# Kernel tuning notes

Measured on AMD Instinct MI355X. Metric: run time of the kernel, lower is better.

Reference implementation:

```python
import jax, jax.numpy as jnp
import numpy as np

N = 100000   # nodes
E = 1600000  # edges
D = 128      # input feature dim
H = 64       # hidden dim
G = 64       # graphs in batch


def setup_inputs() -> dict:
    key = jax.random.key(0)
    ks = jax.random.split(key, 12)
    x = jax.random.normal(ks[0], (N, D), dtype=jnp.float32)
    ei = jax.random.randint(ks[1], (2, E), 0, N, dtype=jnp.int32)
    ew = jax.random.uniform(ks[2], (E,), dtype=jnp.float32)
    b = jnp.sort(jax.random.randint(ks[3], (N,), 0, G, dtype=jnp.int32))
    s = 0.05
    W1 = jax.random.normal(ks[4], (D, H), jnp.float32) * s
    b1 = jnp.zeros((H,), jnp.float32)
    W2 = jax.random.normal(ks[5], (H, H), jnp.float32) * s
    b2 = jnp.zeros((H,), jnp.float32)
    Wm1 = jax.random.normal(ks[6], (H, 32), jnp.float32) * s
    bm1 = jnp.zeros((32,), jnp.float32)
    Wm2 = jax.random.normal(ks[7], (32, 1), jnp.float32) * s
    bm2 = jnp.zeros((1,), jnp.float32)
    return {"x": x, "ei": ei, "ew": ew, "b": b,
            "W1": W1, "b1": b1, "W2": W2, "b2": b2,
            "Wm1": Wm1, "bm1": bm1, "Wm2": Wm2, "bm2": bm2}


def _gcn_norm(ei, ew, n):
    # PyG gcn_norm with add_self_loops=True (self-loop weight 1)
    loops = jnp.arange(n, dtype=ei.dtype)
    row = jnp.concatenate([ei[0], loops])
    col = jnp.concatenate([ei[1], loops])
    w = jnp.concatenate([ew, jnp.ones((n,), ew.dtype)])
    deg = jax.ops.segment_sum(w, col, num_segments=n)
    dinv = jnp.where(deg > 0, jax.lax.rsqrt(deg), 0.0)
    norm = dinv[row] * w * dinv[col]  # [E+N]
    return row, col, norm


def _gcn_conv(x, W, bias, row, col, norm, n):
    h = x @ W                                   # [N,H] small GEMM
    msg = h[row] * norm[:, None]                # gather over edges
    return jax.ops.segment_sum(msg, col, num_segments=n) + bias


def reference(x, ei, ew, b, W1, b1, W2, b2, Wm1, bm1, Wm2, bm2):
    n = x.shape[0]
    row, col, norm = _gcn_norm(ei, ew, n)
    h = jax.nn.relu(_gcn_conv(x, W1, b1, row, col, norm, n))
    h = jax.nn.relu(_gcn_conv(h, W2, b2, row, col, norm, n))
    # global_mean_pool over batch vector b
    sums = jax.ops.segment_sum(h, b, num_segments=G)
    cnt = jax.ops.segment_sum(jnp.ones((n,), h.dtype), b, num_segments=G)
    pooled = sums / jnp.maximum(cnt, 1.0)[:, None]  # [G,H]
    # MLP head: Linear(H,32) -> ReLU -> Linear(32,1)
    return jax.nn.relu(pooled @ Wm1 + bm1) @ Wm2 + bm2
```

## Files before the change

kernel.cpp:

```cpp
#include <hip/hip_runtime.h>
#include <hip/hip_bf16.h>
#include <hip/hip_fp16.h>


#define DIMH 64
#define BSH 7
#define BSZ 128
#define NBUCK_MAX 1024
#define EPB 4096
#define ESTRIDE 3072
#define CSTRIDE 4096

typedef _Float16 v8h __attribute__((ext_vector_type(8)));
typedef _Float16 v4h __attribute__((ext_vector_type(4)));
typedef _Float16 hv2 __attribute__((ext_vector_type(2)));
typedef float v4f __attribute__((ext_vector_type(4)));

__global__ __launch_bounds__(512) void k_part(const int* __restrict__ row,
                                              const int* __restrict__ col,
                                              const float* __restrict__ ew,
                                              int* __restrict__ cursor,
                                              unsigned long long* __restrict__ part,
                                              int E, int nbuck) {
    __shared__ int h[NBUCK_MAX];
    __shared__ int h2[NBUCK_MAX];
    __shared__ int st[NBUCK_MAX];
    for (int i = threadIdx.x; i < nbuck; i += 512) { h[i] = 0; h2[i] = 0; }
    __syncthreads();
    int ebeg = blockIdx.x * EPB;
    int eend = min(ebeg + EPB, E);
    for (int e = ebeg + threadIdx.x; e < eend; e += 512)
        atomicAdd(&h[col[e] >> BSH], 1);
    __syncthreads();
    for (int i = threadIdx.x; i < nbuck; i += 512) {
        int c = h[i];
        st[i] = c ? i * ESTRIDE + atomicAdd(&cursor[i], c) : 0;
    }
    __syncthreads();
    for (int e = ebeg + threadIdx.x; e < eend; e += 512) {
        int c = col[e];
        int b = c >> BSH;
        int r = atomicAdd(&h2[b], 1);
        int slot = st[b] + r;
        if (slot < (b + 1) * ESTRIDE) {
            unsigned long long rec =
                ((unsigned long long)__float_as_uint(ew[e]) << 32) |
                ((unsigned long long)(unsigned)row[e] << 8) |
                (unsigned)(c & (BSZ - 1));
            part[slot] = rec;
        }
    }
}

__global__ __launch_bounds__(256) void k_sortB(const unsigned long long* __restrict__ part,
                                               const int* __restrict__ cursor,
                                               int2* __restrict__ csr,
                                               unsigned* __restrict__ rp,
                                               float* __restrict__ dinv, int N) {
    __shared__ int cnt[BSZ];
    __shared__ int scn[BSZ];
    __shared__ int cur[BSZ];
    __shared__ float dg[BSZ];
    int b = blockIdx.x;
    int nb0 = b << BSH;
    int nn = min(BSZ, N - nb0);
    int tid = threadIdx.x;
    if (tid < BSZ) { cnt[tid] = 0; dg[tid] = 1.0f; }
    __syncthreads();
    int ebeg = b * ESTRIDE;
    int eend = ebeg + min(cursor[b], ESTRIDE);
    for (int e = ebeg + tid; e < eend; e += 256)
        atomicAdd(&cnt[(int)(part[e] & (BSZ - 1))], 1);
    __syncthreads();
    int pc = 0;
    if (tid < BSZ) pc = min((cnt[tid] + 15) & ~15, 496);
    if (tid < BSZ) scn[tid] = pc;
    __syncthreads();
    for (int o = 1; o < BSZ; o <<= 1) {
        int t = 0;
        if (tid >= o && tid < BSZ) t = scn[tid - o];
        __syncthreads();
        if (tid >= o && tid < BSZ) scn[tid] += t;
        __syncthreads();
    }
    int Pb = b * CSTRIDE;
    int pofs = 0;
    if (tid < BSZ) {
        pofs = scn[tid] - pc;
        cur[tid] = pofs;
        if (tid < nn)
            rp[nb0 + tid] = ((unsigned)(pc >> 4) << 26) | (unsigned)(Pb + pofs);
    }
    __syncthreads();
    for (int e = ebeg + tid; e < eend; e += 256) {
        unsigned long long rec = part[e];
        int cl = (int)(rec & (BSZ - 1));
        float w = __uint_as_float((unsigned)(rec >> 32));
        int slot = atomicAdd(&cur[cl], 1);
        csr[Pb + slot] = make_int2((int)((rec >> 8) & 0xFFFFFF), __float_as_int(w));
        atomicAdd(&dg[cl], w);
    }
    __syncthreads();
    if (tid < nn) {
        int c = min(cnt[tid], pc);
        for (int k = c; k < pc; k++)
            csr[Pb + pofs + k] = make_int2(nb0 + tid, 0);
        dinv[nb0 + tid] = rsqrtf(dg[tid]);
    }
}

__global__ __launch_bounds__(256) void k_gemm_mfma(const float* __restrict__ X,
                                                   const float* __restrict__ W,
                                                   const float* __restrict__ dinv,
                                                   __half* __restrict__ Y, int n) {
    __shared__ _Float16 Wh[128 * 64];
    int tid = threadIdx.x;
    for (int i = tid * 4; i < 128 * 64; i += 256 * 4) {
        float4 w = *(const float4*)&W[i];
        Wh[i]     = (_Float16)w.x;
        Wh[i + 1] = (_Float16)w.y;
        Wh[i + 2] = (_Float16)w.z;
        Wh[i + 3] = (_Float16)w.w;
    }
    __syncthreads();

    int wv = tid >> 6;
    int lane = tid & 63;
    int m = lane & 15;
    int quad = lane >> 4;
    int tile = blockIdx.x * 4 + wv;
    int ntiles = (n + 15) >> 4;
    if (tile >= ntiles) return;

    v8h bf[4][4];
#pragma unroll
    for (int nt = 0; nt < 4; nt++)
#pragma unroll
        for (int s = 0; s < 4; s++)
#pragma unroll
            for (int j = 0; j < 8; j++)
                bf[nt][s][j] = Wh[(s * 32 + quad * 8 + j) * 64 + nt * 16 + m];

    v4f acc[4];
#pragma unroll
    for (int nt = 0; nt < 4; nt++) acc[nt] = (v4f){0.f, 0.f, 0.f, 0.f};

    int row = min(tile * 16 + m, n - 1);
    const float* xr = X + (size_t)row * 128;
#pragma unroll
    for (int s = 0; s < 4; s++) {
        float4 lo = *(const float4*)&xr[s * 32 + quad * 8];
        float4 hi = *(const float4*)&xr[s * 32 + quad * 8 + 4];
        v8h af;
        af[0] = (_Float16)lo.x; af[1] = (_Float16)lo.y;
        af[2] = (_Float16)lo.z; af[3] = (_Float16)lo.w;
        af[4] = (_Float16)hi.x; af[5] = (_Float16)hi.y;
        af[6] = (_Float16)hi.z; af[7] = (_Float16)hi.w;
#pragma unroll
        for (int nt = 0; nt < 4; nt++)
            acc[nt] = __builtin_amdgcn_mfma_f32_16x16x32_f16(af, bf[nt][s], acc[nt], 0, 0, 0);
    }

#pragma unroll
    for (int r = 0; r < 4; r++) {
        int node = tile * 16 + quad * 4 + r;
        if (node < n) {
            float di = dinv[node];
#pragma unroll
            for (int nt = 0; nt < 4; nt++)
                Y[(size_t)node * DIMH + nt * 16 + m] = __float2half(di * acc[nt][r]);
        }
    }
}

__global__ __launch_bounds__(256, 8) void k_agg1f(const __half* __restrict__ Hin,
                                                  const unsigned* __restrict__ rp,
                                                  const int2* __restrict__ csr,
                                                  const float* __restrict__ dinv,
                                                  const float* __restrict__ bias,
                                                  const float* __restrict__ W2,
                                                  __half* __restrict__ T2, int n) {
    __shared__ __align__(16) _Float16 W2T[64 * 68];
    __shared__ __align__(16) _Float16 hbuf[4][DIMH];
    int tid = threadIdx.x;
    for (int idx = tid; idx < 64 * 64; idx += 256) {
        int k = idx >> 6;
        int o = idx & 63;
        W2T[o * 68 + k] = (_Float16)W2[idx];
    }
    __syncthreads();

    int lane = tid & 63;
    int wv = tid >> 6;
    int q = lane >> 4;
    int fp = lane & 15;

    const char* Hb = (const char*)Hin;
    const char* Cb = (const char*)csr;
    int ngroups = (n + 3) >> 2;
    for (int grp = blockIdx.x; grp < ngroups; grp += gridDim.x) {
        int node = grp * 4 + wv;
        if (node >= n) continue;
        unsigned pk = rp[node];
        unsigned pb = ((pk & 0x3FFFFFFu) << 3) + (unsigned)(q << 4);
        int iters = (int)(pk >> 26);
        float a0 = 0.f, a1 = 0.f, a2 = 0.f, a3 = 0.f;
        if (q == 0) {
            uint2 su = *(const uint2*)(Hb + (((unsigned)node << 7) + (unsigned)(fp << 3)));
            float2 f0 = __half22float2(*(__half2*)&su.x);
            float2 f1 = __half22float2(*(__half2*)&su.y);
            a0 = f0.x; a1 = f0.y; a2 = f1.x; a3 = f1.y;
        }
        unsigned fo = (unsigned)(fp << 3);
        int it = 0;
        for (; it + 2 <= iters; it += 2, pb += 256) {
            int4 mA0 = *(const int4*)(Cb + pb);
            int4 mB0 = *(const int4*)(Cb + pb + 64);
            int4 mA1 = *(const int4*)(Cb + pb + 128);
            int4 mB1 = *(const int4*)(Cb + pb + 192);
            uint2 u0 = *(const uint2*)(Hb + (((unsigned)mA0.x << 7) + fo));
            uint2 u1 = *(const uint2*)(Hb + (((unsigned)mA0.z << 7) + fo));
            uint2 u2 = *(const uint2*)(Hb + (((unsigned)mB0.x << 7) + fo));
            uint2 u3 = *(const uint2*)(Hb + (((unsigned)mB0.z << 7) + fo));
            uint2 u4 = *(const uint2*)(Hb + (((unsigned)mA1.x << 7) + fo));
            uint2 u5 = *(const uint2*)(Hb + (((unsigned)mA1.z << 7) + fo));
            uint2 u6 = *(const uint2*)(Hb + (((unsigned)mB1.x << 7) + fo));
            uint2 u7 = *(const uint2*)(Hb + (((unsigned)mB1.z << 7) + fo));
            float w0 = __int_as_float(mA0.y), w1 = __int_as_float(mA0.w);
            float w2 = __int_as_float(mB0.y), w3 = __int_as_float(mB0.w);
            float w4 = __int_as_float(mA1.y), w5 = __int_as_float(mA1.w);
            float w6 = __int_as_float(mB1.y), w7 = __int_as_float(mB1.w);
            float2 f;
            f = __half22float2(*(__half2*)&u0.x); a0 += w0 * f.x; a1 += w0 * f.y;
            f = __half22float2(*(__half2*)&u0.y); a2 += w0 * f.x; a3 += w0 * f.y;
            f = __half22float2(*(__half2*)&u1.x); a0 += w1 * f.x; a1 += w1 * f.y;
            f = __half22float2(*(__half2*)&u1.y); a2 += w1 * f.x; a3 += w1 * f.y;
            f = __half22float2(*(__half2*)&u2.x); a0 += w2 * f.x; a1 += w2 * f.y;
            f = __half22float2(*(__half2*)&u2.y); a2 += w2 * f.x; a3 += w2 * f.y;
            f = __half22float2(*(__half2*)&u3.x); a0 += w3 * f.x; a1 += w3 * f.y;
            f = __half22float2(*(__half2*)&u3.y); a2 += w3 * f.x; a3 += w3 * f.y;
            f = __half22float2(*(__half2*)&u4.x); a0 += w4 * f.x; a1 += w4 * f.y;
            f = __half22float2(*(__half2*)&u4.y); a2 += w4 * f.x; a3 += w4 * f.y;
            f = __half22float2(*(__half2*)&u5.x); a0 += w5 * f.x; a1 += w5 * f.y;
            f = __half22float2(*(__half2*)&u5.y); a2 += w5 * f.x; a3 += w5 * f.y;
            f = __half22float2(*(__half2*)&u6.x); a0 += w6 * f.x; a1 += w6 * f.y;
            f = __half22float2(*(__half2*)&u6.y); a2 += w6 * f.x; a3 += w6 * f.y;
            f = __half22float2(*(__half2*)&u7.x); a0 += w7 * f.x; a1 += w7 * f.y;
            f = __half22float2(*(__half2*)&u7.y); a2 += w7 * f.x; a3 += w7 * f.y;
        }
        if (it < iters) {
            int4 mA = *(const int4*)(Cb + pb);
            int4 mB = *(const int4*)(Cb + pb + 64);
            uint2 u0 = *(const uint2*)(Hb + (((unsigned)mA.x << 7) + fo));
            uint2 u1 = *(const uint2*)(Hb + (((unsigned)mA.z << 7) + fo));
            uint2 u2 = *(const uint2*)(Hb + (((unsigned)mB.x << 7) + fo));
            uint2 u3 = *(const uint2*)(Hb + (((unsigned)mB.z << 7) + fo));
            float w0 = __int_as_float(mA.y), w1 = __int_as_float(mA.w);
            float w2 = __int_as_float(mB.y), w3 = __int_as_float(mB.w);
            float2 f;
            f = __half22float2(*(__half2*)&u0.x); a0 += w0 * f.x; a1 += w0 * f.y;
            f = __half22float2(*(__half2*)&u0.y); a2 += w0 * f.x; a3 += w0 * f.y;
            f = __half22float2(*(__half2*)&u1.x); a0 += w1 * f.x; a1 += w1 * f.y;
            f = __half22float2(*(__half2*)&u1.y); a2 += w1 * f.x; a3 += w1 * f.y;
            f = __half22float2(*(__half2*)&u2.x); a0 += w2 * f.x; a1 += w2 * f.y;
            f = __half22float2(*(__half2*)&u2.y); a2 += w2 * f.x; a3 += w2 * f.y;
            f = __half22float2(*(__half2*)&u3.x); a0 += w3 * f.x; a1 += w3 * f.y;
            f = __half22float2(*(__half2*)&u3.y); a2 += w3 * f.x; a3 += w3 * f.y;
        }
        a0 += __shfl_xor(a0, 16, 64); a0 += __shfl_xor(a0, 32, 64);
        a1 += __shfl_xor(a1, 16, 64); a1 += __shfl_xor(a1, 32, 64);
        a2 += __shfl_xor(a2, 16, 64); a2 += __shfl_xor(a2, 32, 64);
        a3 += __shfl_xor(a3, 16, 64); a3 += __shfl_xor(a3, 32, 64);
        float di = dinv[node];
        if (q == 0) {
            float4 bs = *(const float4*)&bias[fp * 4];
            float v0 = fmaxf(di * a0 + bs.x, 0.f);
            float v1 = fmaxf(di * a1 + bs.y, 0.f);
            float v2 = fmaxf(di * a2 + bs.z, 0.f);
            float v3 = fmaxf(di * a3 + bs.w, 0.f);
            __half2 h0 = __floats2half2_rn(v0, v1);
            __half2 h1 = __floats2half2_rn(v2, v3);
            uint2 o;
            o.x = *(unsigned*)&h0;
            o.y = *(unsigned*)&h1;
            *(uint2*)&hbuf[wv][fp * 4] = o;
        }
        float accA = 0.f, accB = 0.f;
#pragma unroll
        for (int k8 = 0; k8 < 8; k8++) {
            v8h hv = *(const v8h*)&hbuf[wv][k8 * 8];
            v4h wa = *(const v4h*)&W2T[lane * 68 + k8 * 8];
            v4h wb = *(const v4h*)&W2T[lane * 68 + k8 * 8 + 4];
            hv2 h0 = {hv[0], hv[1]}, h1 = {hv[2], hv[3]};
            hv2 h2_ = {hv[4], hv[5]}, h3 = {hv[6], hv[7]};
            hv2 w0 = {wa[0], wa[1]}, w1 = {wa[2], wa[3]};
            hv2 w2_ = {wb[0], wb[1]}, w3 = {wb[2], wb[3]};
            accA = __builtin_amdgcn_fdot2(h0, w0, accA, false);
            accB = __builtin_amdgcn_fdot2(h1, w1, accB, false);
            accA = __builtin_amdgcn_fdot2(h2_, w2_, accA, false);
            accB = __builtin_amdgcn_fdot2(h3, w3, accB, false);
        }
        T2[(size_t)node * DIMH + lane] = __float2half(di * (accA + accB));
    }
}

__global__ __launch_bounds__(256, 8) void k_aggN(const __half* __restrict__ Hin,
                                                 const unsigned* __restrict__ rp,
                                                 const int2* __restrict__ csr,
                                                 const float* __restrict__ dinv,
                                                 const float* __restrict__ bias,
                                                 __half* __restrict__ Hout, int n) {
    int lane = threadIdx.x & 63;
    int wv = threadIdx.x >> 6;
    int node = blockIdx.x * 4 + wv;
    if (node >= n) return;
    unsigned pk = rp[node];
    int iters = (int)(pk >> 26);
    int q = lane >> 4;
    int fp = lane & 15;
    unsigned pb = ((pk & 0x3FFFFFFu) << 3) + (unsigned)(q << 4);
    unsigned fo = (unsigned)(fp << 3);
    const char* Hb = (const char*)Hin;
    const char* Cb = (const char*)csr;
    float a0 = 0.f, a1 = 0.f, a2 = 0.f, a3 = 0.f;
    if (q == 0) {
        uint2 su = *(const uint2*)(Hb + (((unsigned)node << 7) + fo));
        float2 f0 = __half22float2(*(__half2*)&su.x);
        float2 f1 = __half22float2(*(__half2*)&su.y);
        a0 = f0.x; a1 = f0.y; a2 = f1.x; a3 = f1.y;
    }
    int it = 0;
    for (; it + 2 <= iters; it += 2, pb += 256) {
        int4 mA0 = *(const int4*)(Cb + pb);
        int4 mB0 = *(const int4*)(Cb + pb + 64);
        int4 mA1 = *(const int4*)(Cb + pb + 128);
        int4 mB1 = *(const int4*)(Cb + pb + 192);
        uint2 u0 = *(const uint2*)(Hb + (((unsigned)mA0.x << 7) + fo));
        uint2 u1 = *(const uint2*)(Hb + (((unsigned)mA0.z << 7) + fo));
        uint2 u2 = *(const uint2*)(Hb + (((unsigned)mB0.x << 7) + fo));
        uint2 u3 = *(const uint2*)(Hb + (((unsigned)mB0.z << 7) + fo));
        uint2 u4 = *(const uint2*)(Hb + (((unsigned)mA1.x << 7) + fo));
        uint2 u5 = *(const uint2*)(Hb + (((unsigned)mA1.z << 7) + fo));
        uint2 u6 = *(const uint2*)(Hb + (((unsigned)mB1.x << 7) + fo));
        uint2 u7 = *(const uint2*)(Hb + (((unsigned)mB1.z << 7) + fo));
        float w0 = __int_as_float(mA0.y), w1 = __int_as_float(mA0.w);
        float w2 = __int_as_float(mB0.y), w3 = __int_as_float(mB0.w);
        float w4 = __int_as_float(mA1.y), w5 = __int_as_float(mA1.w);
        float w6 = __int_as_float(mB1.y), w7 = __int_as_float(mB1.w);
        float2 f;
        f = __half22float2(*(__half2*)&u0.x); a0 += w0 * f.x; a1 += w0 * f.y;
        f = __half22float2(*(__half2*)&u0.y); a2 += w0 * f.x; a3 += w0 * f.y;
        f = __half22float2(*(__half2*)&u1.x); a0 += w1 * f.x; a1 += w1 * f.y;
        f = __half22float2(*(__half2*)&u1.y); a2 += w1 * f.x; a3 += w1 * f.y;
        f = __half22float2(*(__half2*)&u2.x); a0 += w2 * f.x; a1 += w2 * f.y;
        f = __half22float2(*(__half2*)&u2.y); a2 += w2 * f.x; a3 += w2 * f.y;
        f = __half22float2(*(__half2*)&u3.x); a0 += w3 * f.x; a1 += w3 * f.y;
        f = __half22float2(*(__half2*)&u3.y); a2 += w3 * f.x; a3 += w3 * f.y;
        f = __half22float2(*(__half2*)&u4.x); a0 += w4 * f.x; a1 += w4 * f.y;
        f = __half22float2(*(__half2*)&u4.y); a2 += w4 * f.x; a3 += w4 * f.y;
        f = __half22float2(*(__half2*)&u5.x); a0 += w5 * f.x; a1 += w5 * f.y;
        f = __half22float2(*(__half2*)&u5.y); a2 += w5 * f.x; a3 += w5 * f.y;
        f = __half22float2(*(__half2*)&u6.x); a0 += w6 * f.x; a1 += w6 * f.y;
        f = __half22float2(*(__half2*)&u6.y); a2 += w6 * f.x; a3 += w6 * f.y;
        f = __half22float2(*(__half2*)&u7.x); a0 += w7 * f.x; a1 += w7 * f.y;
        f = __half22float2(*(__half2*)&u7.y); a2 += w7 * f.x; a3 += w7 * f.y;
    }
    if (it < iters) {
        int4 mA = *(const int4*)(Cb + pb);
        int4 mB = *(const int4*)(Cb + pb + 64);
        uint2 u0 = *(const uint2*)(Hb + (((unsigned)mA.x << 7) + fo));
        uint2 u1 = *(const uint2*)(Hb + (((unsigned)mA.z << 7) + fo));
        uint2 u2 = *(const uint2*)(Hb + (((unsigned)mB.x << 7) + fo));
        uint2 u3 = *(const uint2*)(Hb + (((unsigned)mB.z << 7) + fo));
        float w0 = __int_as_float(mA.y), w1 = __int_as_float(mA.w);
        float w2 = __int_as_float(mB.y), w3 = __int_as_float(mB.w);
        float2 f;
        f = __half22float2(*(__half2*)&u0.x); a0 += w0 * f.x; a1 += w0 * f.y;
        f = __half22float2(*(__half2*)&u0.y); a2 += w0 * f.x; a3 += w0 * f.y;
        f = __half22float2(*(__half2*)&u1.x); a0 += w1 * f.x; a1 += w1 * f.y;
        f = __half22float2(*(__half2*)&u1.y); a2 += w1 * f.x; a3 += w1 * f.y;
        f = __half22float2(*(__half2*)&u2.x); a0 += w2 * f.x; a1 += w2 * f.y;
        f = __half22float2(*(__half2*)&u2.y); a2 += w2 * f.x; a3 += w2 * f.y;
        f = __half22float2(*(__half2*)&u3.x); a0 += w3 * f.x; a1 += w3 * f.y;
        f = __half22float2(*(__half2*)&u3.y); a2 += w3 * f.x; a3 += w3 * f.y;
    }
    a0 += __shfl_xor(a0, 16, 64); a0 += __shfl_xor(a0, 32, 64);
    a1 += __shfl_xor(a1, 16, 64); a1 += __shfl_xor(a1, 32, 64);
    a2 += __shfl_xor(a2, 16, 64); a2 += __shfl_xor(a2, 32, 64);
    a3 += __shfl_xor(a3, 16, 64); a3 += __shfl_xor(a3, 32, 64);
    if (q == 0) {
        float di = dinv[node];
        float4 bs = *(const float4*)&bias[fp * 4];
        float v0 = fmaxf(di * a0 + bs.x, 0.f);
        float v1 = fmaxf(di * a1 + bs.y, 0.f);
        float v2 = fmaxf(di * a2 + bs.z, 0.f);
        float v3 = fmaxf(di * a3 + bs.w, 0.f);
        __half2 h0 = __floats2half2_rn(v0, v1);
        __half2 h1 = __floats2half2_rn(v2, v3);
        uint2 o;
        o.x = *(unsigned*)&h0;
        o.y = *(unsigned*)&h1;
        *(uint2*)&Hout[(size_t)node * DIMH + fp * 4] = o;
    }
}

__global__ __launch_bounds__(256) void k_pool(const __half* __restrict__ Hin,
                                              const int* __restrict__ b,
                                              float* __restrict__ sums,
                                              float* __restrict__ cntG, int n) {
    const int CHUNK = 64;
    int lane = threadIdx.x & 63;
    int wave = threadIdx.x >> 6;
    int start = (blockIdx.x * 4 + wave) * CHUNK;
    if (start >= n) return;
    int end = min(start + CHUNK, n);
    float acc = 0.f;
    int g_cur = b[start];
    int cnt_local = 0;
    for (int i = start; i < end; i++) {
        int g = b[i];
        if (g != g_cur) {
            atomicAdd(&sums[g_cur * DIMH + lane], acc);
            if (lane == 0) atomicAdd(&cntG[g_cur], (float)cnt_local);
            acc = 0.f;
            cnt_local = 0;
            g_cur = g;
        }
        acc += __half2float(Hin[(size_t)i * DIMH + lane]);
        cnt_local++;
    }
    atomicAdd(&sums[g_cur * DIMH + lane], acc);
    if (lane == 0) atomicAdd(&cntG[g_cur], (float)cnt_local);
}

__global__ __launch_bounds__(64) void k_mlp(const float* __restrict__ sums,
                                            const float* __restrict__ cntG,
                                            const float* __restrict__ Wm1,
                                            const float* __restrict__ bm1,
                                            const float* __restrict__ Wm2,
                                            const float* __restrict__ bm2,
                                            float* __restrict__ out, int G) {
    int g = threadIdx.x;
    if (g >= G) return;
    float c = cntG[g];
    float inv = 1.f / (c > 1.f ? c : 1.f);
    float pooled[DIMH];
#pragma unroll
    for (int k = 0; k < DIMH; k++) pooled[k] = sums[g * DIMH + k] * inv;
    float o = 0.f;
    for (int j = 0; j < 32; j++) {
        float t = bm1[j];
#pragma unroll
        for (int k = 0; k < DIMH; k++) t += pooled[k] * Wm1[k * 32 + j];
        t = t > 0.f ? t : 0.f;
        o += t * Wm2[j];
    }
    out[g] = o + bm2[0];
}


extern "C" void kernel_launch(void* const* d_in, const int* in_sizes, int n_in,
                              void* d_out, int out_size, void* d_ws, size_t ws_size,
                              hipStream_t stream) {
    const float* x   = (const float*)d_in[0];
    const int*   ei  = (const int*)d_in[1];
    const float* ew  = (const float*)d_in[2];
    const int*   bvec= (const int*)d_in[3];
    const float* W1  = (const float*)d_in[4];
    const float* b1  = (const float*)d_in[5];
    const float* W2  = (const float*)d_in[6];
    const float* b2  = (const float*)d_in[7];
    const float* Wm1 = (const float*)d_in[8];
    const float* bm1 = (const float*)d_in[9];
    const float* Wm2 = (const float*)d_in[10];
    const float* bm2 = (const float*)d_in[11];
    float* out = (float*)d_out;

    const int E = in_sizes[2];
    const int N = in_sizes[3];
    const int G = out_size;
    const int* row = ei;
    const int* col = ei + E;
    const int nbuck = (N + BSZ - 1) >> BSH;

    char* p = (char*)d_ws;
    auto alloc = [&](size_t bytes) {
        void* r = (void*)p;
        p += (bytes + 255) & ~(size_t)255;
        return r;
    };

    unsigned long long* part = (unsigned long long*)alloc((size_t)nbuck * ESTRIDE * 8);
    int2*  csr    = (int2*)alloc((size_t)nbuck * CSTRIDE * 8);
    unsigned* rp  = (unsigned*)alloc((size_t)N * 4);
    float* dinv   = (float*)alloc((size_t)N * 4);
    __half* hA    = (__half*)alloc((size_t)N * DIMH * 2);
    __half* hB    = (__half*)alloc((size_t)N * DIMH * 2);
    int zeroInts  = nbuck + G * DIMH + G;
    int* cursor   = (int*)alloc((size_t)zeroInts * 4);
    float* sums   = (float*)(cursor + nbuck);
    float* cntG   = sums + G * DIMH;

    hipMemsetAsync(cursor, 0, (size_t)zeroInts * 4, stream);

    const int PB = (E + EPB - 1) / EPB;
    const int NT = (N + 15) / 16;

    k_part<<<PB, 512, 0, stream>>>(row, col, ew, cursor, part, E, nbuck);
    k_sortB<<<nbuck, 256, 0, stream>>>(part, cursor, csr, rp, dinv, N);

    k_gemm_mfma<<<(NT + 3) / 4, 256, 0, stream>>>(x, W1, dinv, hA, N);

    k_agg1f<<<4096, 256, 0, stream>>>(hA, rp, csr, dinv, b1, W2, hB, N);

    k_aggN<<<(N + 3) / 4, 256, 0, stream>>>(hB, rp, csr, dinv, b2, hA, N);

    k_pool<<<(N + 255) / 256, 256, 0, stream>>>(hA, bvec, sums, cntG, N);
    k_mlp<<<1, 64, 0, stream>>>(sums, cntG, Wm1, bm1, Wm2, bm2, out, G);
}
```

Before: 312.6 us.

## Split layer-2 features into four column planes and aggregate each plane separately

k_agg1f now writes the transformed layer-2 features in a planar layout: four 16-feature planes of 32-byte rows instead of 128-byte rows. The second aggregation kernel launches a 4-wide grid in y, one plane per y index, and each wave gathers 32-byte chunks with 16 edge groups of 4 lanes. The aim is for each plane (3.2 MB) to fit in cache so the random gathers hit better. In exchange the CSR edge list is read four times, and there are two more shuffle-reduction stages and smaller per-lane gathers.

```diff
diff --git a/kernel.cpp b/kernel.cpp
--- a/kernel.cpp
+++ b/kernel.cpp
@@ -300,97 +300,71 @@
             accA = __builtin_amdgcn_fdot2(h2_, w2_, accA, false);
             accB = __builtin_amdgcn_fdot2(h3, w3, accB, false);
         }
-        T2[(size_t)node * DIMH + lane] = __float2half(di * (accA + accB));
-    }
-}
-
-__global__ __launch_bounds__(256, 8) void k_aggN(const __half* __restrict__ Hin,
-                                                 const unsigned* __restrict__ rp,
-                                                 const int2* __restrict__ csr,
-                                                 const float* __restrict__ dinv,
-                                                 const float* __restrict__ bias,
-                                                 __half* __restrict__ Hout, int n) {
+        unsigned tofs = ((((unsigned)q * (unsigned)n + (unsigned)node) << 5)
+                         + ((unsigned)fp << 1));
+        *(__half*)((char*)T2 + tofs) = __float2half(di * (accA + accB));
+    }
+}
+
+__global__ __launch_bounds__(256, 8) void k_aggNc(const __half* __restrict__ T2p,
+                                                  const unsigned* __restrict__ rp,
+                                                  const int2* __restrict__ csr,
+                                                  const float* __restrict__ dinv,
+                                                  const float* __restrict__ bias,
+                                                  __half* __restrict__ Hout, int n) {
     int lane = threadIdx.x & 63;
     int wv = threadIdx.x >> 6;
     int node = blockIdx.x * 4 + wv;
     if (node >= n) return;
+    int c = blockIdx.y;
+    int g = lane >> 2;
+    int t = lane & 3;
     unsigned pk = rp[node];
     int iters = (int)(pk >> 26);
-    int q = lane >> 4;
-    int fp = lane & 15;
-    unsigned pb = ((pk & 0x3FFFFFFu) << 3) + (unsigned)(q << 4);
-    unsigned fo = (unsigned)(fp << 3);
-    const char* Hb = (const char*)Hin;
+    unsigned pb = ((pk & 0x3FFFFFFu) << 3) + ((unsigned)g << 3);
+    unsigned plane = (unsigned)c * (unsigned)n;
+    unsigned to = (unsigned)t << 3;
+    const char* Hb = (const char*)T2p;
     const char* Cb = (const char*)csr;
     float a0 = 0.f, a1 = 0.f, a2 = 0.f, a3 = 0.f;
-    if (q == 0) {
-        uint2 su = *(const uint2*)(Hb + (((unsigned)node << 7) + fo));
+    if (g == 0) {
+        uint2 su = *(const uint2*)(Hb + (((plane + (unsigned)node) << 5) + to));
         float2 f0 = __half22float2(*(__half2*)&su.x);
         float2 f1 = __half22float2(*(__half2*)&su.y);
         a0 = f0.x; a1 = f0.y; a2 = f1.x; a3 = f1.y;
     }
     int it = 0;
     for (; it + 2 <= iters; it += 2, pb += 256) {
-        int4 mA0 = *(const int4*)(Cb + pb);
-        int4 mB0 = *(const int4*)(Cb + pb + 64);
-        int4 mA1 = *(const int4*)(Cb + pb + 128);
-        int4 mB1 = *(const int4*)(Cb + pb + 192);
-        uint2 u0 = *(const uint2*)(Hb + (((unsigned)mA0.x << 7) + fo));
-        uint2 u1 = *(const uint2*)(Hb + (((unsigned)mA0.z << 7) + fo));
-        uint2 u2 = *(const uint2*)(Hb + (((unsigned)mB0.x << 7) + fo));
-        uint2 u3 = *(const uint2*)(Hb + (((unsigned)mB0.z << 7) + fo));
-        uint2 u4 = *(const uint2*)(Hb + (((unsigned)mA1.x << 7) + fo));
-        uint2 u5 = *(const uint2*)(Hb + (((unsigned)mA1.z << 7) + fo));
-        uint2 u6 = *(const uint2*)(Hb + (((unsigned)mB1.x << 7) + fo));
-        uint2 u7 = *(const uint2*)(Hb + (((unsigned)mB1.z << 7) + fo));
-        float w0 = __int_as_float(mA0.y), w1 = __int_as_float(mA0.w);
-        float w2 = __int_as_float(mB0.y), w3 = __int_as_float(mB0.w);
-        float w4 = __int_as_float(mA1.y), w5 = __int_as_float(mA1.w);
-        float w6 = __int_as_float(mB1.y), w7 = __int_as_float(mB1.w);
+        uint2 r0 = *(const uint2*)(Cb + pb);
+        uint2 r1 = *(const uint2*)(Cb + pb + 128);
+        uint2 u0 = *(const uint2*)(Hb + (((plane + r0.x) << 5) + to));
+        uint2 u1 = *(const uint2*)(Hb + (((plane + r1.x) << 5) + to));
+        float w0 = __uint_as_float(r0.y), w1 = __uint_as_float(r1.y);
         float2 f;
         f = __half22float2(*(__half2*)&u0.x); a0 += w0 * f.x; a1 += w0 * f.y;
         f = __half22float2(*(__half2*)&u0.y); a2 += w0 * f.x; a3 += w0 * f.y;
         f = __half22float2(*(__half2*)&u1.x); a0 += w1 * f.x; a1 += w1 * f.y;
         f = __half22float2(*(__half2*)&u1.y); a2 += w1 * f.x; a3 += w1 * f.y;
-        f = __half22float2(*(__half2*)&u2.x); a0 += w2 * f.x; a1 += w2 * f.y;
-        f = __half22float2(*(__half2*)&u2.y); a2 += w2 * f.x; a3 += w2 * f.y;
-        f = __half22float2(*(__half2*)&u3.x); a0 += w3 * f.x; a1 += w3 * f.y;
-        f = __half22float2(*(__half2*)&u3.y); a2 += w3 * f.x; a3 += w3 * f.y;
-        f = __half22float2(*(__half2*)&u4.x); a0 += w4 * f.x; a1 += w4 * f.y;
-        f = __half22float2(*(__half2*)&u4.y); a2 += w4 * f.x; a3 += w4 * f.y;
-        f = __half22float2(*(__half2*)&u5.x); a0 += w5 * f.x; a1 += w5 * f.y;
-        f = __half22float2(*(__half2*)&u5.y); a2 += w5 * f.x; a3 += w5 * f.y;
-        f = __half22float2(*(__half2*)&u6.x); a0 += w6 * f.x; a1 += w6 * f.y;
-        f = __half22float2(*(__half2*)&u6.y); a2 += w6 * f.x; a3 += w6 * f.y;
-        f = __half22float2(*(__half2*)&u7.x); a0 += w7 * f.x; a1 += w7 * f.y;
-        f = __half22float2(*(__half2*)&u7.y); a2 += w7 * f.x; a3 += w7 * f.y;
     }
     if (it < iters) {
-        int4 mA = *(const int4*)(Cb + pb);
-        int4 mB = *(const int4*)(Cb + pb + 64);
-        uint2 u0 = *(const uint2*)(Hb + (((unsigned)mA.x << 7) + fo));
-        uint2 u1 = *(const uint2*)(Hb + (((unsigned)mA.z << 7) + fo));
-        uint2 u2 = *(const uint2*)(Hb + (((unsigned)mB.x << 7) + fo));
-        uint2 u3 = *(const uint2*)(Hb + (((unsigned)mB.z << 7) + fo));
-        float w0 = __int_as_float(mA.y), w1 = __int_as_float(mA.w);
-        float w2 = __int_as_float(mB.y), w3 = __int_as_float(mB.w);
+        uint2 r0 = *(const uint2*)(Cb + pb);
+        uint2 u0 = *(const uint2*)(Hb + (((plane + r0.x) << 5) + to));
+        float w0 = __uint_as_float(r0.y);
         float2 f;
         f = __half22float2(*(__half2*)&u0.x); a0 += w0 * f.x; a1 += w0 * f.y;
         f = __half22float2(*(__half2*)&u0.y); a2 += w0 * f.x; a3 += w0 * f.y;
-        f = __half22float2(*(__half2*)&u1.x); a0 += w1 * f.x; a1 += w1 * f.y;
-        f = __half22float2(*(__half2*)&u1.y); a2 += w1 * f.x; a3 += w1 * f.y;
-        f = __half22float2(*(__half2*)&u2.x); a0 += w2 * f.x; a1 += w2 * f.y;
-        f = __half22float2(*(__half2*)&u2.y); a2 += w2 * f.x; a3 += w2 * f.y;
-        f = __half22float2(*(__half2*)&u3.x); a0 += w3 * f.x; a1 += w3 * f.y;
-        f = __half22float2(*(__half2*)&u3.y); a2 += w3 * f.x; a3 += w3 * f.y;
-    }
+    }
+    a0 += __shfl_xor(a0, 4, 64); a0 += __shfl_xor(a0, 8, 64);
     a0 += __shfl_xor(a0, 16, 64); a0 += __shfl_xor(a0, 32, 64);
+    a1 += __shfl_xor(a1, 4, 64); a1 += __shfl_xor(a1, 8, 64);
     a1 += __shfl_xor(a1, 16, 64); a1 += __shfl_xor(a1, 32, 64);
+    a2 += __shfl_xor(a2, 4, 64); a2 += __shfl_xor(a2, 8, 64);
     a2 += __shfl_xor(a2, 16, 64); a2 += __shfl_xor(a2, 32, 64);
+    a3 += __shfl_xor(a3, 4, 64); a3 += __shfl_xor(a3, 8, 64);
     a3 += __shfl_xor(a3, 16, 64); a3 += __shfl_xor(a3, 32, 64);
-    if (q == 0) {
+    if (g == 0) {
         float di = dinv[node];
-        float4 bs = *(const float4*)&bias[fp * 4];
+        float4 bs = *(const float4*)&bias[c * 16 + t * 4];
         float v0 = fmaxf(di * a0 + bs.x, 0.f);
         float v1 = fmaxf(di * a1 + bs.y, 0.f);
         float v2 = fmaxf(di * a2 + bs.z, 0.f);
@@ -400,7 +374,7 @@
         uint2 o;
         o.x = *(unsigned*)&h0;
         o.y = *(unsigned*)&h1;
-        *(uint2*)&Hout[(size_t)node * DIMH + fp * 4] = o;
+        *(uint2*)&Hout[(size_t)node * DIMH + c * 16 + t * 4] = o;
     }
 }
 
@@ -505,6 +479,7 @@
 
     const int PB = (E + EPB - 1) / EPB;
     const int NT = (N + 15) / 16;
+    const int NG = (N + 3) / 4;
 
     k_part<<<PB, 512, 0, stream>>>(row, col, ew, cursor, part, E, nbuck);
     k_sortB<<<nbuck, 256, 0, stream>>>(part, cursor, csr, rp, dinv, N);
@@ -513,7 +488,7 @@
 
     k_agg1f<<<4096, 256, 0, stream>>>(hA, rp, csr, dinv, b1, W2, hB, N);
 
-    k_aggN<<<(N + 3) / 4, 256, 0, stream>>>(hB, rp, csr, dinv, b2, hA, N);
+    k_aggNc<<<dim3(NG, 4), 256, 0, stream>>>(hB, rp, csr, dinv, b2, hA, N);
 
     k_pool<<<(N + 255) / 256, 256, 0, stream>>>(hA, bvec, sums, cntG, N);
     k_mlp<<<1, 64, 0, stream>>>(sums, cntG, Wm1, bm1, Wm2, bm2, out, G);
```

New measurement: 373.6 us. +19.5%, slower.

## Pad CSR rows to 8 instead of 16 and cache edge records in registers

Applied to the files above, without the earlier changes.

Per-node CSR padding granularity drops from 16 to 8 edges, so the aggregation kernels gather fewer dummy padded edges. The gather loops are reorganized into 4-group, 2-group and 1-group tails to match the finer granularity. The partition and sort kernels also keep the column indices and records they read in the first pass in registers, instead of re-reading them from global memory in the second pass. This adds register pressure and fixed-size per-thread arrays that assume bounded per-thread counts.

```diff
diff --git a/kernel.cpp b/kernel.cpp
--- a/kernel.cpp
+++ b/kernel.cpp
@@ -29,16 +29,22 @@
     __syncthreads();
     int ebeg = blockIdx.x * EPB;
     int eend = min(ebeg + EPB, E);
-    for (int e = ebeg + threadIdx.x; e < eend; e += 512)
-        atomicAdd(&h[col[e] >> BSH], 1);
+    int myc[8];
+    int m = 0;
+    for (int e = ebeg + threadIdx.x; e < eend; e += 512) {
+        int c = col[e];
+        myc[m++] = c;
+        atomicAdd(&h[c >> BSH], 1);
+    }
     __syncthreads();
     for (int i = threadIdx.x; i < nbuck; i += 512) {
         int c = h[i];
         st[i] = c ? i * ESTRIDE + atomicAdd(&cursor[i], c) : 0;
     }
     __syncthreads();
-    for (int e = ebeg + threadIdx.x; e < eend; e += 512) {
-        int c = col[e];
+    m = 0;
+    for (int e = ebeg + threadIdx.x; e < eend; e += 512, m++) {
+        int c = myc[m];
         int b = c >> BSH;
         int r = atomicAdd(&h2[b], 1);
         int slot = st[b] + r;
@@ -69,11 +75,16 @@
     __syncthreads();
     int ebeg = b * ESTRIDE;
     int eend = ebeg + min(cursor[b], ESTRIDE);
-    for (int e = ebeg + tid; e < eend; e += 256)
-        atomicAdd(&cnt[(int)(part[e] & (BSZ - 1))], 1);
+    unsigned long long myrec[12];
+    int nrec = 0;
+    for (int e = ebeg + tid; e < eend; e += 256) {
+        unsigned long long rec = part[e];
+        myrec[nrec++] = rec;
+        atomicAdd(&cnt[(int)(rec & (BSZ - 1))], 1);
+    }
     __syncthreads();
     int pc = 0;
-    if (tid < BSZ) pc = min((cnt[tid] + 15) & ~15, 496);
+    if (tid < BSZ) pc = min((cnt[tid] + 7) & ~7, 496);
     if (tid < BSZ) scn[tid] = pc;
     __syncthreads();
     for (int o = 1; o < BSZ; o <<= 1) {
@@ -89,11 +100,11 @@
         pofs = scn[tid] - pc;
         cur[tid] = pofs;
         if (tid < nn)
-            rp[nb0 + tid] = ((unsigned)(pc >> 4) << 26) | (unsigned)(Pb + pofs);
-    }
-    __syncthreads();
-    for (int e = ebeg + tid; e < eend; e += 256) {
-        unsigned long long rec = part[e];
+            rp[nb0 + tid] = ((unsigned)(pc >> 3) << 26) | (unsigned)(Pb + pofs);
+    }
+    __syncthreads();
+    for (int i = 0; i < nrec; i++) {
+        unsigned long long rec = myrec[i];
         int cl = (int)(rec & (BSZ - 1));
         float w = __uint_as_float((unsigned)(rec >> 32));
         int slot = atomicAdd(&cur[cl], 1);
@@ -203,7 +214,7 @@
         if (node >= n) continue;
         unsigned pk = rp[node];
         unsigned pb = ((pk & 0x3FFFFFFu) << 3) + (unsigned)(q << 4);
-        int iters = (int)(pk >> 26);
+        int g8 = (int)(pk >> 26);
         float a0 = 0.f, a1 = 0.f, a2 = 0.f, a3 = 0.f;
         if (q == 0) {
             uint2 su = *(const uint2*)(Hb + (((unsigned)node << 7) + (unsigned)(fp << 3)));
@@ -213,7 +224,7 @@
         }
         unsigned fo = (unsigned)(fp << 3);
         int it = 0;
-        for (; it + 2 <= iters; it += 2, pb += 256) {
+        for (; it + 4 <= g8; it += 4, pb += 256) {
             int4 mA0 = *(const int4*)(Cb + pb);
             int4 mB0 = *(const int4*)(Cb + pb + 64);
             int4 mA1 = *(const int4*)(Cb + pb + 128);
@@ -248,7 +259,7 @@
             f = __half22float2(*(__half2*)&u7.x); a0 += w7 * f.x; a1 += w7 * f.y;
             f = __half22float2(*(__half2*)&u7.y); a2 += w7 * f.x; a3 += w7 * f.y;
         }
-        if (it < iters) {
+        if (it + 2 <= g8) {
             int4 mA = *(const int4*)(Cb + pb);
             int4 mB = *(const int4*)(Cb + pb + 64);
             uint2 u0 = *(const uint2*)(Hb + (((unsigned)mA.x << 7) + fo));
@@ -266,6 +277,18 @@
             f = __half22float2(*(__half2*)&u2.y); a2 += w2 * f.x; a3 += w2 * f.y;
             f = __half22float2(*(__half2*)&u3.x); a0 += w3 * f.x; a1 += w3 * f.y;
             f = __half22float2(*(__half2*)&u3.y); a2 += w3 * f.x; a3 += w3 * f.y;
+            pb += 128; it += 2;
+        }
+        if (it < g8) {
+            int4 mA = *(const int4*)(Cb + pb);
+            uint2 u0 = *(const uint2*)(Hb + (((unsigned)mA.x << 7) + fo));
+            uint2 u1 = *(const uint2*)(Hb + (((unsigned)mA.z << 7) + fo));
+            float w0 = __int_as_float(mA.y), w1 = __int_as_float(mA.w);
+            float2 f;
+            f = __half22float2(*(__half2*)&u0.x); a0 += w0 * f.x; a1 += w0 * f.y;
+            f = __half22float2(*(__half2*)&u0.y); a2 += w0 * f.x; a3 += w0 * f.y;
+            f = __half22float2(*(__half2*)&u1.x); a0 += w1 * f.x; a1 += w1 * f.y;
+            f = __half22float2(*(__half2*)&u1.y); a2 += w1 * f.x; a3 += w1 * f.y;
         }
         a0 += __shfl_xor(a0, 16, 64); a0 += __shfl_xor(a0, 32, 64);
         a1 += __shfl_xor(a1, 16, 64); a1 += __shfl_xor(a1, 32, 64);
@@ -315,7 +338,7 @@
     int node = blockIdx.x * 4 + wv;
     if (node >= n) return;
     unsigned pk = rp[node];
-    int iters = (int)(pk >> 26);
+    int g8 = (int)(pk >> 26);
     int q = lane >> 4;
     int fp = lane & 15;
     unsigned pb = ((pk & 0x3FFFFFFu) << 3) + (unsigned)(q << 4);
@@ -330,7 +353,7 @@
         a0 = f0.x; a1 = f0.y; a2 = f1.x; a3 = f1.y;
     }
     int it = 0;
-    for (; it + 2 <= iters; it += 2, pb += 256) {
+    for (; it + 4 <= g8; it += 4, pb += 256) {
         int4 mA0 = *(const int4*)(Cb + pb);
         int4 mB0 = *(const int4*)(Cb + pb + 64);
         int4 mA1 = *(const int4*)(Cb + pb + 128);
@@ -365,7 +388,7 @@
         f = __half22float2(*(__half2*)&u7.x); a0 += w7 * f.x; a1 += w7 * f.y;
         f = __half22float2(*(__half2*)&u7.y); a2 += w7 * f.x; a3 += w7 * f.y;
     }
-    if (it < iters) {
+    if (it + 2 <= g8) {
         int4 mA = *(const int4*)(Cb + pb);
         int4 mB = *(const int4*)(Cb + pb + 64);
         uint2 u0 = *(const uint2*)(Hb + (((unsigned)mA.x << 7) + fo));
@@ -383,6 +406,18 @@
         f = __half22float2(*(__half2*)&u2.y); a2 += w2 * f.x; a3 += w2 * f.y;
         f = __half22float2(*(__half2*)&u3.x); a0 += w3 * f.x; a1 += w3 * f.y;
         f = __half22float2(*(__half2*)&u3.y); a2 += w3 * f.x; a3 += w3 * f.y;
+        pb += 128; it += 2;
+    }
+    if (it < g8) {
+        int4 mA = *(const int4*)(Cb + pb);
+        uint2 u0 = *(const uint2*)(Hb + (((unsigned)mA.x << 7) + fo));
+        uint2 u1 = *(const uint2*)(Hb + (((unsigned)mA.z << 7) + fo));
+        float w0 = __int_as_float(mA.y), w1 = __int_as_float(mA.w);
+        float2 f;
+        f = __half22float2(*(__half2*)&u0.x); a0 += w0 * f.x; a1 += w0 * f.y;
+        f = __half22float2(*(__half2*)&u0.y); a2 += w0 * f.x; a3 += w0 * f.y;
+        f = __half22float2(*(__half2*)&u1.x); a0 += w1 * f.x; a1 += w1 * f.y;
+        f = __half22float2(*(__half2*)&u1.y); a2 += w1 * f.x; a3 += w1 * f.y;
     }
     a0 += __shfl_xor(a0, 16, 64); a0 += __shfl_xor(a0, 32, 64);
     a1 += __shfl_xor(a1, 16, 64); a1 += __shfl_xor(a1, 32, 64);
```

Result: no change. 307.1 us (median of 2 runs) (-1.8%).
